# Kernel tuning notes

Measured on AMD Instinct MI355X. Metric: run time of the kernel, lower is better.

The kernel has to match this reference:

```python
import jax, jax.numpy as jnp
import numpy as np

B, S, H = 4, 2048, 768
NUM_HEADS = 12
HEAD_DIM = H // NUM_HEADS


def setup_inputs() -> dict:
    key = jax.random.key(0)
    k1, k2, k3 = jax.random.split(key, 3)
    hidden_states = jax.random.normal(k1, (B, S, H), dtype=jnp.float32)
    # torch Linear weight [out,in]; store transposed [in,out] for x @ W
    w_qkv = jax.random.normal(k2, (H, 3 * H), dtype=jnp.float32) * (1.0 / np.sqrt(H))
    w_out = jax.random.normal(k3, (H, H), dtype=jnp.float32) * (1.0 / np.sqrt(H))
    return {"hidden_states": hidden_states, "w_qkv": w_qkv, "w_out": w_out}


def reference(hidden_states, w_qkv, w_out):
    b, s, h = hidden_states.shape
    qkv = hidden_states @ w_qkv                      # [b,s,3h]
    qkv = qkv.reshape(b, s, 3, NUM_HEADS, HEAD_DIM)
    qkv = jnp.transpose(qkv, (2, 0, 3, 1, 4))        # [3,b,nh,s,hd]
    q, k, v = qkv[0], qkv[1], qkv[2]
    scale = 1.0 / np.sqrt(HEAD_DIM).astype(np.float32)
    scores = jnp.einsum('bhqd,bhkd->bhqk', q, k) * scale   # [b,nh,s,s]
    causal = jnp.triu(jnp.ones((s, s), dtype=bool), k=1)
    scores = jnp.where(causal, jnp.float32(-jnp.inf), scores)
    attn = jax.nn.softmax(scores, axis=-1)
    # dropout is identity in eval mode
    out = jnp.einsum('bhqk,bhkd->bhqd', attn, v)      # [b,nh,s,hd]
    out = jnp.transpose(out, (0, 2, 1, 3)).reshape(b, s, h)
    return out @ w_out
```

## Files before the change

### kernel.cpp

```cpp
#include <hip/hip_runtime.h>
#include <stdint.h>

#define B_ 4
#define S_ 2048
#define H_ 768
#define NH_ 12
#define HD_ 64
#define BH_ (B_ * NH_)

typedef __attribute__((ext_vector_type(4))) float f32x4;
typedef __attribute__((ext_vector_type(8))) __bf16 bf16x8;
typedef __attribute__((ext_vector_type(8))) unsigned short ushort8;
typedef __attribute__((ext_vector_type(4))) unsigned short ushort4v;

__device__ __forceinline__ unsigned short bf16rne(float f) {
  union { float f; unsigned int u; } v;
  v.f = f;
  unsigned int u = v.u;
  return (unsigned short)((u + 0x7fffu + ((u >> 16) & 1u)) >> 16);
}

__device__ __forceinline__ void gll16(const void* g, void* l) {
  __builtin_amdgcn_global_load_lds(
      (const __attribute__((address_space(1))) unsigned int*)g,
      (__attribute__((address_space(3))) unsigned int*)l, 16, 0, 0);
}

__global__ __launch_bounds__(256) void cvt_bf16_kernel(const float* __restrict__ x,
                                                       unsigned short* __restrict__ y) {
  int i = (blockIdx.x * 256 + threadIdx.x) * 8;
  const float4* p = (const float4*)(x + i);
  float4 a = p[0], b = p[1];
  ushort8 r;
  r[0] = bf16rne(a.x); r[1] = bf16rne(a.y); r[2] = bf16rne(a.z); r[3] = bf16rne(a.w);
  r[4] = bf16rne(b.x); r[5] = bf16rne(b.y); r[6] = bf16rne(b.z); r[7] = bf16rne(b.w);
  *(ushort8*)(y + i) = r;
}

__global__ __launch_bounds__(256) void tconv_kernel(const float* __restrict__ in,
                                                    unsigned short* __restrict__ out,
                                                    int R, int C) {
  __shared__ unsigned short tile[64][72];
  int c0 = blockIdx.x * 64, r0 = blockIdx.y * 64;
  int tid = threadIdx.x;
#pragma unroll
  for (int i = 0; i < 4; ++i) {
    int c = i * 256 + tid;
    int row = c >> 4, col4 = (c & 15) * 4;
    float4 v = *(const float4*)(in + (size_t)(r0 + row) * C + c0 + col4);
    tile[row][col4 + 0] = bf16rne(v.x);
    tile[row][col4 + 1] = bf16rne(v.y);
    tile[row][col4 + 2] = bf16rne(v.z);
    tile[row][col4 + 3] = bf16rne(v.w);
  }
  __syncthreads();
#pragma unroll
  for (int i = 0; i < 2; ++i) {
    int c = i * 256 + tid;
    int oc = c >> 3, r8 = (c & 7) * 8;
    ushort8 v;
#pragma unroll
    for (int j = 0; j < 8; ++j) v[j] = tile[r8 + j][oc];
    *(ushort8*)(out + (size_t)(c0 + oc) * R + r0 + r8) = v;
  }
}

template <int MODE>
__global__ __launch_bounds__(256) void gemm_bt(const unsigned short* __restrict__ A,
                                               const unsigned short* __restrict__ Bm,
                                               void* __restrict__ Cout, int N, int K,
                                               int bn_off) {
  __shared__ unsigned short As[128 * 32];
  __shared__ unsigned short Bs[128 * 32];
  int tid = threadIdx.x;
  int lane = tid & 63, wave = tid >> 6;
  int quad = lane >> 4, l16 = lane & 15;
  int wm = (wave & 1) * 64, wn = (wave >> 1) * 64;
  int bm = blockIdx.x, bn = blockIdx.y + bn_off;
  const unsigned short* Ag = A + (size_t)bm * 128 * K;
  const unsigned short* Bg = Bm + (size_t)bn * 128 * K;

  f32x4 zero = {0.f, 0.f, 0.f, 0.f};
  f32x4 acc[4][4];
#pragma unroll
  for (int mt = 0; mt < 4; ++mt)
#pragma unroll
    for (int nt = 0; nt < 4; ++nt) acc[mt][nt] = zero;

  for (int k0 = 0; k0 < K; k0 += 32) {
#pragma unroll
    for (int i = 0; i < 2; ++i) {
      int c = i * 256 + tid;
      int row = c >> 2, off = (c & 3) * 8;
      gll16(Ag + (size_t)row * K + k0 + off, As + c * 8);
      gll16(Bg + (size_t)row * K + k0 + off, Bs + c * 8);
    }
    __syncthreads();
    bf16x8 af[4], bf[4];
#pragma unroll
    for (int mt = 0; mt < 4; ++mt)
      af[mt] = *(const bf16x8*)(As + (wm + mt * 16 + l16) * 32 + quad * 8);
#pragma unroll
    for (int nt = 0; nt < 4; ++nt)
      bf[nt] = *(const bf16x8*)(Bs + (wn + nt * 16 + l16) * 32 + quad * 8);
#pragma unroll
    for (int mt = 0; mt < 4; ++mt)
#pragma unroll
      for (int nt = 0; nt < 4; ++nt) {
        if (MODE == 2)
          acc[mt][nt] = __builtin_amdgcn_mfma_f32_16x16x32_bf16(af[mt], bf[nt], acc[mt][nt], 0, 0, 0);
        else
          acc[mt][nt] = __builtin_amdgcn_mfma_f32_16x16x32_bf16(bf[nt], af[mt], acc[mt][nt], 0, 0, 0);
      }
    __syncthreads();
  }

  if (MODE == 0) {
    unsigned short* qkv = (unsigned short*)Cout;
    int which = (bn >= 6);
#pragma unroll
    for (int mt = 0; mt < 4; ++mt)
#pragma unroll
      for (int nt = 0; nt < 4; ++nt) {
        int f0 = bn * 128 + wn + nt * 16 + quad * 4;
        int tm = bm * 128 + wm + mt * 16 + l16;
        int rem = f0 - which * 768;
        int head = rem >> 6, d0 = rem & 63;
        int b = tm >> 11, s = tm & 2047;
        ushort4v pk;
        if (which == 0) {
#pragma unroll
          for (int r = 0; r < 4; ++r) pk[r] = bf16rne(acc[mt][nt][r] * 0.125f);
          *(ushort4v*)(qkv + (((size_t)b * NH_ + head) * S_ + s) * HD_ + d0) = pk;
        } else {
#pragma unroll
          for (int r = 0; r < 4; ++r) pk[r] = bf16rne(acc[mt][nt][r]);
          int dd0 = (((d0 >> 3) ^ (s & 7)) << 3) | (d0 & 7);
          *(ushort4v*)(qkv + (((size_t)(BH_ + b * NH_ + head)) * S_ + s) * HD_ + dd0) = pk;
        }
      }
  } else if (MODE == 2) {
    unsigned short* vt = (unsigned short*)Cout;
#pragma unroll
    for (int mt = 0; mt < 4; ++mt)
#pragma unroll
      for (int nt = 0; nt < 4; ++nt) {
        int f = bn * 128 + wn + nt * 16 + l16;
        int t0 = bm * 128 + wm + mt * 16 + quad * 4;
        int rem = f - 1536;
        int head = rem >> 6, d = rem & 63;
        int b = t0 >> 11, s0 = t0 & 2047;
        int tile = s0 >> 6, sin = s0 & 63;
        int pos = (((sin >> 3) ^ (d & 7)) << 3) | (sin & 7);
        ushort4v pk;
#pragma unroll
        for (int r = 0; r < 4; ++r) pk[r] = bf16rne(acc[mt][nt][r]);
        *(ushort4v*)(vt + (((size_t)(b * NH_ + head)) * HD_ + d) * S_ + tile * 64 + pos) = pk;
      }
  } else {
    float* outp = (float*)Cout;
#pragma unroll
    for (int mt = 0; mt < 4; ++mt)
#pragma unroll
      for (int nt = 0; nt < 4; ++nt) {
        int f0 = bn * 128 + wn + nt * 16 + quad * 4;
        int tm = bm * 128 + wm + mt * 16 + l16;
        *(f32x4*)(outp + (size_t)tm * N + f0) = acc[mt][nt];
      }
  }
}

__global__ __launch_bounds__(512, 6) void attn_kernel(const unsigned short* __restrict__ Q,
                                                      const unsigned short* __restrict__ Kg,
                                                      const unsigned short* __restrict__ Vt,
                                                      unsigned short* __restrict__ O) {
  __shared__ unsigned short Ks[2][64 * 64];
  __shared__ unsigned short Vs[2][64 * 64];
  __shared__ unsigned short Ps[8][16 * 64];
  int bh = blockIdx.x;
  int y = blockIdx.y;
  int qt = (y & 1) ? (15 - (y >> 1)) : (y >> 1);
  int tid = threadIdx.x, lane = tid & 63, wave = tid >> 6;
  int quad = lane >> 4, l16 = lane & 15;
  const unsigned short* Qp = Q + (size_t)bh * S_ * HD_;
  const unsigned short* Kp = Kg + (size_t)bh * S_ * HD_;
  const unsigned short* Vp = Vt + (size_t)bh * HD_ * S_;
  int q0 = qt * 128;
  int qrow = q0 + wave * 16 + l16;
  int kmax_w = (q0 + wave * 16 + 15) >> 6;
  int kmax_b = 2 * qt + 1;

  auto stage = [&](int t, int buf) {
    int row = tid >> 3, off = (tid & 7) * 8;
    gll16(Kp + (size_t)t * 64 * HD_ + row * HD_ + off, &Ks[buf][tid * 8]);
    gll16(Vp + (size_t)row * S_ + t * 64 + off, &Vs[buf][tid * 8]);
  };

  stage(0, 0);

  bf16x8 qf[2];
#pragma unroll
  for (int ks = 0; ks < 2; ++ks)
    qf[ks] = *(const bf16x8*)(Qp + (size_t)qrow * HD_ + ks * 32 + quad * 8);

  bf16x8 ones;
#pragma unroll
  for (int j = 0; j < 8; ++j) ones[j] = (__bf16)1.0f;

  f32x4 zero = {0.f, 0.f, 0.f, 0.f};
  float m_i = -1e30f, l_i = 0.f;
  f32x4 o[4];
#pragma unroll
  for (int nt = 0; nt < 4; ++nt) o[nt] = zero;

  for (int t = 0; t <= kmax_b; ++t) {
    __syncthreads();
    if (t < kmax_b) stage(t + 1, (t + 1) & 1);
    if (t > kmax_w) continue;
    const unsigned short* Kb = Ks[t & 1];
    const unsigned short* Vb = Vs[t & 1];

    f32x4 sf[4];
#pragma unroll
    for (int nt = 0; nt < 4; ++nt) sf[nt] = zero;
#pragma unroll
    for (int ks = 0; ks < 2; ++ks)
#pragma unroll
      for (int nt = 0; nt < 4; ++nt) {
        bf16x8 kf = *(const bf16x8*)(Kb + (nt * 16 + l16) * 64 + (((ks * 4 + quad) ^ (l16 & 7)) << 3));
        sf[nt] = __builtin_amdgcn_mfma_f32_16x16x32_bf16(kf, qf[ks], sf[nt], 0, 0, 0);
      }

    if (t == kmax_w) {
#pragma unroll
      for (int nt = 0; nt < 4; ++nt)
#pragma unroll
        for (int r = 0; r < 4; ++r)
          if (t * 64 + nt * 16 + quad * 4 + r > qrow) sf[nt][r] = -1e30f;
    }

    float mx = fmaxf(fmaxf(fmaxf(sf[0][0], sf[0][1]), fmaxf(sf[0][2], sf[0][3])),
                     fmaxf(fmaxf(sf[1][0], sf[1][1]), fmaxf(sf[1][2], sf[1][3])));
    mx = fmaxf(mx, fmaxf(fmaxf(fmaxf(sf[2][0], sf[2][1]), fmaxf(sf[2][2], sf[2][3])),
                         fmaxf(fmaxf(sf[3][0], sf[3][1]), fmaxf(sf[3][2], sf[3][3]))));
    mx = fmaxf(mx, __shfl_xor(mx, 16));
    mx = fmaxf(mx, __shfl_xor(mx, 32));
    float mn = fmaxf(m_i, mx);
    float alpha = __expf(m_i - mn);
    m_i = mn;

#pragma unroll
    for (int nt = 0; nt < 4; ++nt) {
      ushort4v pk;
#pragma unroll
      for (int r = 0; r < 4; ++r) pk[r] = bf16rne(__expf(sf[nt][r] - mn));
      int kvblk = nt * 2 + (quad >> 1);
      *(ushort4v*)(&Ps[wave][l16 * 64 + (((kvblk ^ (l16 & 7)) << 3) | ((quad & 1) * 4))]) = pk;
    }

#pragma unroll
    for (int nt = 0; nt < 4; ++nt)
#pragma unroll
      for (int r = 0; r < 4; ++r) o[nt][r] *= alpha;

    f32x4 rsv = zero;
#pragma unroll
    for (int ks = 0; ks < 2; ++ks) {
      bf16x8 pf = *(const bf16x8*)(&Ps[wave][l16 * 64 + (((ks * 4 + quad) ^ (l16 & 7)) << 3)]);
      rsv = __builtin_amdgcn_mfma_f32_16x16x32_bf16(ones, pf, rsv, 0, 0, 0);
#pragma unroll
      for (int nt = 0; nt < 4; ++nt) {
        bf16x8 vf = *(const bf16x8*)(Vb + (nt * 16 + l16) * 64 + (((ks * 4 + quad) ^ (l16 & 7)) << 3));
        o[nt] = __builtin_amdgcn_mfma_f32_16x16x32_bf16(vf, pf, o[nt], 0, 0, 0);
      }
    }
    l_i = l_i * alpha + rsv[0];
  }

  float inv = 1.f / l_i;
  int b = bh / NH_, h = bh % NH_;
#pragma unroll
  for (int nt = 0; nt < 4; ++nt) {
    ushort4v pk;
#pragma unroll
    for (int r = 0; r < 4; ++r) pk[r] = bf16rne(o[nt][r] * inv);
    int d0 = nt * 16 + quad * 4;
    *(ushort4v*)(O + ((size_t)b * S_ + qrow) * H_ + h * HD_ + d0) = pk;
  }
}

extern "C" void kernel_launch(void* const* d_in, const int* in_sizes, int n_in,
                              void* d_out, int out_size, void* d_ws, size_t ws_size,
                              hipStream_t stream) {
  (void)in_sizes; (void)n_in; (void)out_size; (void)ws_size;
  const float* hs = (const float*)d_in[0];
  const float* wqkv = (const float*)d_in[1];
  const float* wout = (const float*)d_in[2];
  float* out = (float*)d_out;

  unsigned short* Xbf = (unsigned short*)d_ws;
  unsigned short* Wqkvt = Xbf + (size_t)8192 * 768;
  unsigned short* Woutt = Wqkvt + (size_t)2304 * 768;
  unsigned short* QKV = Woutt + (size_t)768 * 768;
  unsigned short* Vt = QKV + (size_t)2 * BH_ * S_ * HD_;
  unsigned short* Attn = Xbf;

  cvt_bf16_kernel<<<3072, 256, 0, stream>>>(hs, Xbf);
  tconv_kernel<<<dim3(36, 12), 256, 0, stream>>>(wqkv, Wqkvt, 768, 2304);
  tconv_kernel<<<dim3(12, 12), 256, 0, stream>>>(wout, Woutt, 768, 768);
  gemm_bt<0><<<dim3(64, 12), 256, 0, stream>>>(Xbf, Wqkvt, QKV, 2304, 768, 0);
  gemm_bt<2><<<dim3(64, 6), 256, 0, stream>>>(Xbf, Wqkvt, Vt, 2304, 768, 12);
  attn_kernel<<<dim3(48, 16), 512, 0, stream>>>(QKV, QKV + (size_t)BH_ * S_ * HD_, Vt, Attn);
  gemm_bt<1><<<dim3(64, 6), 256, 0, stream>>>(Attn, Woutt, out, 768, 768, 0);
}
```

Baseline: 225.2 us.

## Merge prep and QKV launches, use exp2 softmax and packed bf16 conversion

The three conversion kernels become a single prep kernel, and the two QKV GEMM launches become one grid that branches on block column. This cuts the number of kernel launches from seven to four. The Q scale now folds in log2(e), so the attention softmax can use the hardware exp2 instead of __expf. The scalar bf16 rounding is replaced with a packed two-float conversion builtin, which drops several integer ops per conversion. If the builtin is not available, the code falls back to the old rounding routine.

```diff
diff --git a/kernel.cpp b/kernel.cpp
--- a/kernel.cpp
+++ b/kernel.cpp
@@ -8,6 +8,8 @@
 #define HD_ 64
 #define BH_ (B_ * NH_)
 
+#define QSCALE 0.18033688011112042f
+
 typedef __attribute__((ext_vector_type(4))) float f32x4;
 typedef __attribute__((ext_vector_type(8))) __bf16 bf16x8;
 typedef __attribute__((ext_vector_type(8))) unsigned short ushort8;
@@ -20,38 +22,40 @@
   return (unsigned short)((u + 0x7fffu + ((u >> 16) & 1u)) >> 16);
 }
 
+#if __has_builtin(__builtin_amdgcn_cvt_pk_bf16_f32)
+__device__ __forceinline__ unsigned int pk2(float a, float b) {
+  auto r = __builtin_amdgcn_cvt_pk_bf16_f32(a, b);
+  return *(unsigned int*)&r;
+}
+#else
+__device__ __forceinline__ unsigned int pk2(float a, float b) {
+  return (unsigned int)bf16rne(a) | ((unsigned int)bf16rne(b) << 16);
+}
+#endif
+
+#if __has_builtin(__builtin_amdgcn_exp2f)
+#define EXP2F(x) __builtin_amdgcn_exp2f(x)
+#else
+#define EXP2F(x) exp2f(x)
+#endif
+
 __device__ __forceinline__ void gll16(const void* g, void* l) {
   __builtin_amdgcn_global_load_lds(
       (const __attribute__((address_space(1))) unsigned int*)g,
       (__attribute__((address_space(3))) unsigned int*)l, 16, 0, 0);
 }
 
-__global__ __launch_bounds__(256) void cvt_bf16_kernel(const float* __restrict__ x,
-                                                       unsigned short* __restrict__ y) {
-  int i = (blockIdx.x * 256 + threadIdx.x) * 8;
-  const float4* p = (const float4*)(x + i);
-  float4 a = p[0], b = p[1];
-  ushort8 r;
-  r[0] = bf16rne(a.x); r[1] = bf16rne(a.y); r[2] = bf16rne(a.z); r[3] = bf16rne(a.w);
-  r[4] = bf16rne(b.x); r[5] = bf16rne(b.y); r[6] = bf16rne(b.z); r[7] = bf16rne(b.w);
-  *(ushort8*)(y + i) = r;
-}
-
-__global__ __launch_bounds__(256) void tconv_kernel(const float* __restrict__ in,
-                                                    unsigned short* __restrict__ out,
-                                                    int R, int C) {
-  __shared__ unsigned short tile[64][72];
-  int c0 = blockIdx.x * 64, r0 = blockIdx.y * 64;
-  int tid = threadIdx.x;
+__device__ __forceinline__ void tconv_body(const float* __restrict__ in,
+                                           unsigned short* __restrict__ out,
+                                           int R, int C, int bx, int by,
+                                           unsigned short (*tile)[72], int tid) {
+  int c0 = bx * 64, r0 = by * 64;
 #pragma unroll
   for (int i = 0; i < 4; ++i) {
     int c = i * 256 + tid;
     int row = c >> 4, col4 = (c & 15) * 4;
     float4 v = *(const float4*)(in + (size_t)(r0 + row) * C + c0 + col4);
-    tile[row][col4 + 0] = bf16rne(v.x);
-    tile[row][col4 + 1] = bf16rne(v.y);
-    tile[row][col4 + 2] = bf16rne(v.z);
-    tile[row][col4 + 3] = bf16rne(v.w);
+    *(uint2*)(&tile[row][col4]) = (uint2){pk2(v.x, v.y), pk2(v.z, v.w)};
   }
   __syncthreads();
 #pragma unroll
@@ -65,18 +69,39 @@
   }
 }
 
+__global__ __launch_bounds__(256) void prep_kernel(const float* __restrict__ hs,
+                                                   const float* __restrict__ wqkv,
+                                                   const float* __restrict__ wout,
+                                                   unsigned short* __restrict__ Xbf,
+                                                   unsigned short* __restrict__ Wqkvt,
+                                                   unsigned short* __restrict__ Woutt) {
+  __shared__ unsigned short tile[64][72];
+  int bid = blockIdx.x, tid = threadIdx.x;
+  if (bid < 3072) {
+    int i = (bid * 256 + tid) * 8;
+    const float4* p = (const float4*)(hs + i);
+    float4 a = p[0], b = p[1];
+    uint4 r = {pk2(a.x, a.y), pk2(a.z, a.w), pk2(b.x, b.y), pk2(b.z, b.w)};
+    *(uint4*)(Xbf + i) = r;
+  } else if (bid < 3504) {
+    int idx = bid - 3072;
+    tconv_body(wqkv, Wqkvt, 768, 2304, idx % 36, idx / 36, tile, tid);
+  } else {
+    int idx = bid - 3504;
+    tconv_body(wout, Woutt, 768, 768, idx % 12, idx / 12, tile, tid);
+  }
+}
+
 template <int MODE>
-__global__ __launch_bounds__(256) void gemm_bt(const unsigned short* __restrict__ A,
-                                               const unsigned short* __restrict__ Bm,
-                                               void* __restrict__ Cout, int N, int K,
-                                               int bn_off) {
-  __shared__ unsigned short As[128 * 32];
-  __shared__ unsigned short Bs[128 * 32];
+__device__ __forceinline__ void gemm_core(const unsigned short* __restrict__ A,
+                                          const unsigned short* __restrict__ Bm,
+                                          void* __restrict__ Cout, int N, int K,
+                                          int bm, int bn,
+                                          unsigned short* As, unsigned short* Bs) {
   int tid = threadIdx.x;
   int lane = tid & 63, wave = tid >> 6;
   int quad = lane >> 4, l16 = lane & 15;
   int wm = (wave & 1) * 64, wn = (wave >> 1) * 64;
-  int bm = blockIdx.x, bn = blockIdx.y + bn_off;
   const unsigned short* Ag = A + (size_t)bm * 128 * K;
   const unsigned short* Bg = Bm + (size_t)bn * 128 * K;
 
@@ -127,16 +152,15 @@
         int rem = f0 - which * 768;
         int head = rem >> 6, d0 = rem & 63;
         int b = tm >> 11, s = tm & 2047;
-        ushort4v pk;
         if (which == 0) {
-#pragma unroll
-          for (int r = 0; r < 4; ++r) pk[r] = bf16rne(acc[mt][nt][r] * 0.125f);
-          *(ushort4v*)(qkv + (((size_t)b * NH_ + head) * S_ + s) * HD_ + d0) = pk;
+          uint2 pkv = {pk2(acc[mt][nt][0] * QSCALE, acc[mt][nt][1] * QSCALE),
+                       pk2(acc[mt][nt][2] * QSCALE, acc[mt][nt][3] * QSCALE)};
+          *(uint2*)(qkv + (((size_t)b * NH_ + head) * S_ + s) * HD_ + d0) = pkv;
         } else {
-#pragma unroll
-          for (int r = 0; r < 4; ++r) pk[r] = bf16rne(acc[mt][nt][r]);
+          uint2 pkv = {pk2(acc[mt][nt][0], acc[mt][nt][1]),
+                       pk2(acc[mt][nt][2], acc[mt][nt][3])};
           int dd0 = (((d0 >> 3) ^ (s & 7)) << 3) | (d0 & 7);
-          *(ushort4v*)(qkv + (((size_t)(BH_ + b * NH_ + head)) * S_ + s) * HD_ + dd0) = pk;
+          *(uint2*)(qkv + (((size_t)(BH_ + b * NH_ + head)) * S_ + s) * HD_ + dd0) = pkv;
         }
       }
   } else if (MODE == 2) {
@@ -152,10 +176,9 @@
         int b = t0 >> 11, s0 = t0 & 2047;
         int tile = s0 >> 6, sin = s0 & 63;
         int pos = (((sin >> 3) ^ (d & 7)) << 3) | (sin & 7);
-        ushort4v pk;
-#pragma unroll
-        for (int r = 0; r < 4; ++r) pk[r] = bf16rne(acc[mt][nt][r]);
-        *(ushort4v*)(vt + (((size_t)(b * NH_ + head)) * HD_ + d) * S_ + tile * 64 + pos) = pk;
+        uint2 pkv = {pk2(acc[mt][nt][0], acc[mt][nt][1]),
+                     pk2(acc[mt][nt][2], acc[mt][nt][3])};
+        *(uint2*)(vt + (((size_t)(b * NH_ + head)) * HD_ + d) * S_ + tile * 64 + pos) = pkv;
       }
   } else {
     float* outp = (float*)Cout;
@@ -168,6 +191,27 @@
         *(f32x4*)(outp + (size_t)tm * N + f0) = acc[mt][nt];
       }
   }
+}
+
+__global__ __launch_bounds__(256) void gemm_qkv(const unsigned short* __restrict__ A,
+                                                const unsigned short* __restrict__ Bm,
+                                                unsigned short* __restrict__ QK,
+                                                unsigned short* __restrict__ Vt) {
+  __shared__ unsigned short As[128 * 32];
+  __shared__ unsigned short Bs[128 * 32];
+  int bm = blockIdx.x, bn = blockIdx.y;
+  if (bn < 12)
+    gemm_core<0>(A, Bm, QK, 2304, 768, bm, bn, As, Bs);
+  else
+    gemm_core<2>(A, Bm, Vt, 2304, 768, bm, bn, As, Bs);
+}
+
+__global__ __launch_bounds__(256) void gemm_out(const unsigned short* __restrict__ A,
+                                                const unsigned short* __restrict__ Bm,
+                                                float* __restrict__ Cout) {
+  __shared__ unsigned short As[128 * 32];
+  __shared__ unsigned short Bs[128 * 32];
+  gemm_core<1>(A, Bm, Cout, 768, 768, blockIdx.x, blockIdx.y, As, Bs);
 }
 
 __global__ __launch_bounds__(512, 6) void attn_kernel(const unsigned short* __restrict__ Q,
@@ -246,16 +290,15 @@
     mx = fmaxf(mx, __shfl_xor(mx, 16));
     mx = fmaxf(mx, __shfl_xor(mx, 32));
     float mn = fmaxf(m_i, mx);
-    float alpha = __expf(m_i - mn);
+    float alpha = EXP2F(m_i - mn);
     m_i = mn;
 
 #pragma unroll
     for (int nt = 0; nt < 4; ++nt) {
-      ushort4v pk;
-#pragma unroll
-      for (int r = 0; r < 4; ++r) pk[r] = bf16rne(__expf(sf[nt][r] - mn));
+      uint2 pkv = {pk2(EXP2F(sf[nt][0] - mn), EXP2F(sf[nt][1] - mn)),
+                   pk2(EXP2F(sf[nt][2] - mn), EXP2F(sf[nt][3] - mn))};
       int kvblk = nt * 2 + (quad >> 1);
-      *(ushort4v*)(&Ps[wave][l16 * 64 + (((kvblk ^ (l16 & 7)) << 3) | ((quad & 1) * 4))]) = pk;
+      *(uint2*)(&Ps[wave][l16 * 64 + (((kvblk ^ (l16 & 7)) << 3) | ((quad & 1) * 4))]) = pkv;
     }
 
 #pragma unroll
@@ -281,11 +324,10 @@
   int b = bh / NH_, h = bh % NH_;
 #pragma unroll
   for (int nt = 0; nt < 4; ++nt) {
-    ushort4v pk;
-#pragma unroll
-    for (int r = 0; r < 4; ++r) pk[r] = bf16rne(o[nt][r] * inv);
+    uint2 pkv = {pk2(o[nt][0] * inv, o[nt][1] * inv),
+                 pk2(o[nt][2] * inv, o[nt][3] * inv)};
     int d0 = nt * 16 + quad * 4;
-    *(ushort4v*)(O + ((size_t)b * S_ + qrow) * H_ + h * HD_ + d0) = pk;
+    *(uint2*)(O + ((size_t)b * S_ + qrow) * H_ + h * HD_ + d0) = pkv;
   }
 }
 
@@ -301,15 +343,12 @@
   unsigned short* Xbf = (unsigned short*)d_ws;
   unsigned short* Wqkvt = Xbf + (size_t)8192 * 768;
   unsigned short* Woutt = Wqkvt + (size_t)2304 * 768;
-  unsigned short* QKV = Woutt + (size_t)768 * 768;
-  unsigned short* Vt = QKV + (size_t)2 * BH_ * S_ * HD_;
+  unsigned short* QK = Woutt + (size_t)768 * 768;
+  unsigned short* Vt = QK + (size_t)2 * BH_ * S_ * HD_;
   unsigned short* Attn = Xbf;
 
-  cvt_bf16_kernel<<<3072, 256, 0, stream>>>(hs, Xbf);
-  tconv_kernel<<<dim3(36, 12), 256, 0, stream>>>(wqkv, Wqkvt, 768, 2304);
-  tconv_kernel<<<dim3(12, 12), 256, 0, stream>>>(wout, Woutt, 768, 768);
-  gemm_bt<0><<<dim3(64, 12), 256, 0, stream>>>(Xbf, Wqkvt, QKV, 2304, 768, 0);
-  gemm_bt<2><<<dim3(64, 6), 256, 0, stream>>>(Xbf, Wqkvt, Vt, 2304, 768, 12);
-  attn_kernel<<<dim3(48, 16), 512, 0, stream>>>(QKV, QKV + (size_t)BH_ * S_ * HD_, Vt, Attn);
-  gemm_bt<1><<<dim3(64, 6), 256, 0, stream>>>(Attn, Woutt, out, 768, 768, 0);
-}
+  prep_kernel<<<3648, 256, 0, stream>>>(hs, wqkv, wout, Xbf, Wqkvt, Woutt);
+  gemm_qkv<<<dim3(64, 18), 256, 0, stream>>>(Xbf, Wqkvt, QK, Vt);
+  attn_kernel<<<dim3(48, 16), 512, 0, stream>>>(QK, QK + (size_t)BH_ * S_ * HD_, Vt, Attn);
+  gemm_out<<<dim3(64, 6), 256, 0, stream>>>(Attn, Woutt, out);
+}
```

Measured after the change: 207.0 us. 8.1% less time.
